# Kernel tuning notes

Measured on AMD Instinct MI355X. Metric: run time of the kernel, lower is better.

## Reference

```python
import jax, jax.numpy as jnp
import numpy as np

B, T, D, L = 64, 512, 400, 25
H = D // 2  # per-direction LSTM hidden


def setup_inputs():
    key = jax.random.key(0)
    ks = jax.random.split(key, 16)
    s = 0.1
    lengths = jax.random.randint(ks[0], (B,), T // 2, T + 1)
    mask = (jnp.arange(T)[None, :] < lengths[:, None]).astype(jnp.float32)
    labels = (jax.random.randint(ks[1], (B, T), 1, L) * mask.astype(jnp.int32)).astype(jnp.int32)

    def n(k, shape):
        return jax.random.normal(k, shape, jnp.float32) * s

    return {
        "input_embed": jax.random.normal(ks[2], (B, T, D), jnp.float32),
        "mask": mask,
        "labels": labels,
        "Wih_f": n(ks[3], (4 * H, D)), "Whh_f": n(ks[4], (4 * H, H)),
        "bih_f": n(ks[5], (4 * H,)), "bhh_f": n(ks[6], (4 * H,)),
        "Wih_b": n(ks[7], (4 * H, D)), "Whh_b": n(ks[8], (4 * H, H)),
        "bih_b": n(ks[9], (4 * H,)), "bhh_b": n(ks[10], (4 * H,)),
        "Wl": n(ks[11], (L, D)), "bl": n(ks[12], (L,)),
        "trans": n(ks[13], (L, L)), "start": n(ks[14], (L,)), "end": n(ks[15], (L,)),
    }


def _lstm_dir(x_tbd, m_tb1, Wih, Whh, bih, bhh, reverse):
    # Masked LSTM scan == pack_padded semantics: state frozen past sequence end.
    Bn = x_tbd.shape[1]
    h0 = jnp.zeros((Bn, H), x_tbd.dtype)

    def step(carry, inp):
        h, c = carry
        x, m = inp
        g = x @ Wih.T + h @ Whh.T + (bih + bhh)
        i, f, gg, o = jnp.split(g, 4, axis=-1)  # PyTorch gate order i,f,g,o
        i, f, o = jax.nn.sigmoid(i), jax.nn.sigmoid(f), jax.nn.sigmoid(o)
        c_new = f * c + i * jnp.tanh(gg)
        h_new = o * jnp.tanh(c_new)
        h = m * h_new + (1.0 - m) * h
        c = m * c_new + (1.0 - m) * c
        return (h, c), h

    _, hs = jax.lax.scan(step, (h0, h0), (x_tbd, m_tb1), reverse=reverse)
    return hs  # [T,B,H]


def _emissions(input_embed, mask, params):
    (Wih_f, Whh_f, bih_f, bhh_f, Wih_b, Whh_b, bih_b, bhh_b, Wl, bl) = params
    x = jnp.transpose(input_embed, (1, 0, 2))    # [T,B,D]
    m = jnp.transpose(mask, (1, 0))[:, :, None]  # [T,B,1]
    hf = _lstm_dir(x, m, Wih_f, Whh_f, bih_f, bhh_f, False)
    hb = _lstm_dir(x, m, Wih_b, Whh_b, bih_b, bhh_b, True)
    h = jnp.concatenate([hf, hb], axis=-1) * m   # pad positions zeroed like pad_packed_sequence
    e = (h @ Wl.T + bl) * m                      # `out *= mask.unsqueeze(-1)`
    return jnp.transpose(e, (1, 0, 2))           # [B,T,L]


def _crf_llh(e, labels, mask, trans, start, end):
    # numerator (gold path score)
    em = jnp.take_along_axis(e, labels[..., None], axis=-1)[..., 0]  # [B,T]
    tr = trans[labels[:, :-1], labels[:, 1:]]                        # [B,T-1]
    last = (jnp.sum(mask, axis=1) - 1.0).astype(jnp.int32)
    y_last = jnp.take_along_axis(labels, last[:, None], axis=1)[:, 0]
    num = start[labels[:, 0]] + em[:, 0] \
        + jnp.sum(mask[:, 1:] * (em[:, 1:] + tr), axis=1) + end[y_last]
    # log-partition via forward algorithm
    e_t = jnp.transpose(e, (1, 0, 2))  # [T,B,L]
    m_t = jnp.transpose(mask, (1, 0))  # [T,B]
    alpha0 = start[None, :] + e_t[0]

    def step(alpha, inp):
        et, mt = inp
        new = jax.nn.logsumexp(alpha[:, :, None] + trans[None], axis=1) + et
        return jnp.where(mt[:, None] > 0, new, alpha), None

    alpha, _ = jax.lax.scan(step, alpha0, (e_t[1:], m_t[1:]))
    logZ = jax.nn.logsumexp(alpha + end[None, :], axis=-1)
    return num - logZ  # [B] log-likelihood


def _viterbi(e, mask, trans, start, end):
    Bn = e.shape[0]
    e_t = jnp.transpose(e, (1, 0, 2))
    m_t = jnp.transpose(mask, (1, 0))
    delta0 = start[None, :] + e_t[0]
    eye_idx = jnp.broadcast_to(jnp.arange(L, dtype=jnp.int32), (Bn, L))

    def step(delta, inp):
        et, mt = inp
        cand = delta[:, :, None] + trans[None]  # [B, L_prev, L_cur]
        ptr = jnp.argmax(cand, axis=1).astype(jnp.int32)
        new = jnp.max(cand, axis=1) + et
        mb = mt[:, None] > 0
        return jnp.where(mb, new, delta), jnp.where(mb, ptr, eye_idx)

    delta, ptrs = jax.lax.scan(step, delta0, (e_t[1:], m_t[1:]))  # ptrs: [T-1,B,L]
    y_last = jnp.argmax(delta + end[None, :], axis=-1).astype(jnp.int32)  # [B]

    def back(y, ptr):
        y_prev = jnp.take_along_axis(ptr, y[:, None], axis=1)[:, 0]
        return y_prev, y_prev

    _, ys = jax.lax.scan(back, y_last, ptrs, reverse=True)  # [T-1,B]
    path = jnp.concatenate([ys, y_last[None]], axis=0)      # [T,B]
    return jnp.transpose(path, (1, 0)) * mask.astype(jnp.int32)  # pads -> pad_idx 0


def reference(input_embed, mask, labels, Wih_f, Whh_f, bih_f, bhh_f,
              Wih_b, Whh_b, bih_b, bhh_b, Wl, bl, trans, start, end):
    params = (Wih_f, Whh_f, bih_f, bhh_f, Wih_b, Whh_b, bih_b, bhh_b, Wl, bl)
    e = _emissions(input_embed, mask, params)
    loss = -jnp.mean(_crf_llh(e, labels, mask, trans, start, end))  # -torch.mean(score)
    preds = _viterbi(e, mask, trans, start, end)
    return loss, preds
```

## Files before the change

kernel.cpp:

```cpp
#include <hip/hip_runtime.h>
#include <cmath>

#define Bn 64
#define Tn 512
#define Dn 400
#define Ln 25
#define Hn 200
#define G4n 800
#define TCn 64
#define NCH 8
#define NPADn 832
#define JV 20
#define JLB 17
#define JSB 3

constexpr size_t OFF_WIHT = 0;
constexpr size_t OFF_WHHP = OFF_WIHT + (size_t)2*Dn*NPADn;
constexpr size_t OFF_WHHB = OFF_WHHP + (size_t)2*Hn*G4n;
constexpr size_t OFF_BSUM = OFF_WHHB + (size_t)2*Hn*G4n/2;
constexpr size_t OFF_GB   = OFF_BSUM + (size_t)2*G4n;
constexpr size_t OFF_HCAT = OFF_GB + (size_t)2*2*Bn*TCn*G4n/2;
constexpr size_t OFF_E    = OFF_HCAT + (size_t)Bn*Tn*2*Hn;
constexpr size_t OFF_HST  = OFF_E + (size_t)Bn*Tn*Ln;
constexpr size_t OFF_CST  = OFF_HST + (size_t)2*Bn*Hn;
constexpr size_t OFF_PART = OFF_CST + (size_t)2*Bn*Hn;

#define SMEM_BYTES 153664

__device__ __forceinline__ float sigf(float x) { return 1.0f / (1.0f + expf(-x)); }

__global__ void prep_kernel(const float* __restrict__ Wih_f, const float* __restrict__ Whh_f,
                            const float* __restrict__ bih_f, const float* __restrict__ bhh_f,
                            const float* __restrict__ Wih_b, const float* __restrict__ Whh_b,
                            const float* __restrict__ bih_b, const float* __restrict__ bhh_b,
                            float* __restrict__ ws) {
    int tid = blockIdx.x * blockDim.x + threadIdx.x;
    int nth = gridDim.x * blockDim.x;
    float* WihT = ws + OFF_WIHT;
    float* WhhP = ws + OFF_WHHP;
    unsigned short* WhhB = (unsigned short*)(ws + OFF_WHHB);
    float* bsum = ws + OFF_BSUM;
    float* hst  = ws + OFF_HST;
    float* cst  = ws + OFF_CST;
    for (int i = tid; i < 2*Dn*NPADn; i += nth) {
        int d = i / (Dn*NPADn); int r = i % (Dn*NPADn); int k = r / NPADn; int g = r % NPADn;
        const float* W = d ? Wih_b : Wih_f;
        WihT[i] = (g < G4n) ? W[(size_t)g*Dn + k] : 0.0f;
    }
    for (int i = tid; i < 2*Hn*G4n; i += nth) {
        int d = i / (Hn*G4n); int r = i % (Hn*G4n);
        int j = r / G4n; int g = r % G4n;
        int k = g >> 2, q = g & 3;
        const float* W = d ? Whh_b : Whh_f;
        float v = W[(size_t)(q*Hn + k)*Hn + j];
        WhhP[i] = v;
        WhhB[i] = (unsigned short)(__float_as_uint(v) >> 16);
    }
    for (int i = tid; i < 2*G4n; i += nth) {
        int d = i / G4n; int g = i % G4n;
        bsum[i] = d ? (bih_b[g] + bhh_b[g]) : (bih_f[g] + bhh_f[g]);
    }
    for (int i = tid; i < 2*Bn*Hn; i += nth) { hst[i] = 0.0f; cst[i] = 0.0f; }
}

__device__ __forceinline__ void gemm_role(const float* __restrict__ X, float* __restrict__ ws,
                                          int chunk, int tile, int tid, char* smem) {
    const float* WihT = ws + OFF_WIHT;
    const float* bsum = ws + OFF_BSUM;
    unsigned short* Gb = (unsigned short*)(ws + OFF_GB) + (size_t)(chunk & 1) * 2 * Bn * TCn * G4n;
    int q4 = tid >> 8;
    int t2 = tid & 255;
    float* As = (float*)(smem + q4 * 13056);
    float* Bs = As + 16 * 136;
    int g0i = tile % 13; int rem = tile / 13;
    int bp = rem % 32;   int d = rem / 32;
    int g0 = g0i * 64;
    int tx = t2 % 16, ty = t2 / 16;
    int t_base = (d == 0) ? chunk * TCn : (Tn - (chunk + 1) * TCn);
    const float* Bmat = WihT + (size_t)d * Dn * NPADn;

    float acc[8][4] = {{0.f}};
    int lr = t2 / 2, lk = t2 % 2;
    int bk = t2 / 16, bg = t2 % 16;
    int a_b = bp * 2 + lr / 64;
    int a_t = t_base + (lr % 64);
    const float* Arow = X + ((size_t)a_b * Tn + a_t) * Dn;

    for (int kt = 0; kt < Dn; kt += 16) {
        float4 a4a = *(const float4*)(Arow + kt + lk * 8);
        float4 a4b = *(const float4*)(Arow + kt + lk * 8 + 4);
        float4 b4  = *(const float4*)(Bmat + (size_t)(kt + bk) * NPADn + g0 + bg * 4);
        __syncthreads();
        As[(lk*8+0)*136 + lr] = a4a.x; As[(lk*8+1)*136 + lr] = a4a.y;
        As[(lk*8+2)*136 + lr] = a4a.z; As[(lk*8+3)*136 + lr] = a4a.w;
        As[(lk*8+4)*136 + lr] = a4b.x; As[(lk*8+5)*136 + lr] = a4b.y;
        As[(lk*8+6)*136 + lr] = a4b.z; As[(lk*8+7)*136 + lr] = a4b.w;
        *(float4*)&Bs[bk*68 + bg*4] = b4;
        __syncthreads();
        #pragma unroll
        for (int kk = 0; kk < 16; ++kk) {
            float4 af0 = *(const float4*)&As[kk*136 + ty*8];
            float4 af1 = *(const float4*)&As[kk*136 + ty*8 + 4];
            float4 bf  = *(const float4*)&Bs[kk*68 + tx*4];
            acc[0][0] += af0.x*bf.x; acc[0][1] += af0.x*bf.y; acc[0][2] += af0.x*bf.z; acc[0][3] += af0.x*bf.w;
            acc[1][0] += af0.y*bf.x; acc[1][1] += af0.y*bf.y; acc[1][2] += af0.y*bf.z; acc[1][3] += af0.y*bf.w;
            acc[2][0] += af0.z*bf.x; acc[2][1] += af0.z*bf.y; acc[2][2] += af0.z*bf.z; acc[2][3] += af0.z*bf.w;
            acc[3][0] += af0.w*bf.x; acc[3][1] += af0.w*bf.y; acc[3][2] += af0.w*bf.z; acc[3][3] += af0.w*bf.w;
            acc[4][0] += af1.x*bf.x; acc[4][1] += af1.x*bf.y; acc[4][2] += af1.x*bf.z; acc[4][3] += af1.x*bf.w;
            acc[5][0] += af1.y*bf.x; acc[5][1] += af1.y*bf.y; acc[5][2] += af1.y*bf.z; acc[5][3] += af1.y*bf.w;
            acc[6][0] += af1.z*bf.x; acc[6][1] += af1.z*bf.y; acc[6][2] += af1.z*bf.z; acc[6][3] += af1.z*bf.w;
            acc[7][0] += af1.w*bf.x; acc[7][1] += af1.w*bf.y; acc[7][2] += af1.w*bf.z; acc[7][3] += af1.w*bf.w;
        }
    }
    #pragma unroll
    for (int ii = 0; ii < 8; ++ii) {
        int r = ty * 8 + ii;
        int b = bp * 2 + r / 64;
        int tloc = r % 64;
        #pragma unroll
        for (int jj = 0; jj < 4; ++jj) {
            int g = g0 + tx * 4 + jj;
            if (g < G4n) {
                int k = g % Hn, q = g / Hn;
                float v = acc[ii][jj] + bsum[d*G4n + g];
                Gb[(((size_t)d*Bn + b)*TCn + tloc)*G4n + k*4 + q] =
                    (unsigned short)(__float_as_uint(v) >> 16);
            }
        }
    }
}

__device__ __forceinline__ void rec_role(const float* __restrict__ mask, float* __restrict__ ws,
                                         int chunk, int b, int d, int tid, char* smem) {
    const unsigned short* Gbs = (const unsigned short*)(ws + OFF_GB) + (size_t)(chunk & 1) * 2 * Bn * TCn * G4n;
    float* Hcat = ws + OFF_HCAT;
    float* hst = ws + OFF_HST;
    float* cst = ws + OFF_CST;
    const float* WP = ws + OFF_WHHP;
    const unsigned short* WBbase = (const unsigned short*)(ws + OFF_WHHB);

    uint2*  wldsB   = (uint2*)smem;
    float4* partial = (float4*)(smem + 136000);
    float*  hbuf    = (float*)(smem + 152000);

    int k = tid % 200;
    int part = tid / 200;
    bool act = (part < 5);
    int cbase = (act ? part : 0) * 40;
    int qq = tid & 3, kk = tid >> 2;
    bool bact = (tid < 800);

    const float* Wd = WP + (size_t)d * Hn * G4n;
    const unsigned short* WB = WBbase + (size_t)d * Hn * G4n;
    #define LW(i) float4 w##i = *(const float4*)(Wd + (size_t)(cbase + i) * G4n + k * 4);
    LW(0) LW(1) LW(2) LW(3) LW(4) LW(5) LW(6) LW(7) LW(8) LW(9)
    LW(10) LW(11) LW(12) LW(13) LW(14) LW(15) LW(16) LW(17) LW(18) LW(19)
    #undef LW
    int lbase = (act ? part : 0) * 200 + k;
    if (act) {
        #pragma unroll
        for (int jj = 0; jj < JLB; ++jj)
            wldsB[jj * 1000 + part * 200 + k] = *(const uint2*)(WB + (size_t)(cbase + JV + jj) * G4n + k * 4);
    }
    size_t soff = ((size_t)d * Bn + b) * Hn;
    float hr = 0.f, cr = 0.f;
    if (bact && qq == 0) {
        hr = hst[soff + kk];
        cr = cst[soff + kk];
    }
    if (tid < 200) hbuf[tid] = hst[soff + tid];
    __syncthreads();

    const unsigned short* WstB = WB + (size_t)(cbase + JV + JLB) * G4n + k * 4;
    const unsigned short* GbRow = Gbs + ((size_t)d * Bn + b) * TCn * G4n;
    const float* mrow = mask + (size_t)b * Tn;
    float* Hrow = Hcat + (size_t)b * Tn * (2 * Hn) + d * Hn;

    #define FMAB(U, H) { \
        float bx = __uint_as_float((U).x << 16); \
        float by = __uint_as_float((U).x & 0xffff0000u); \
        float bz = __uint_as_float((U).y << 16); \
        float bw = __uint_as_float((U).y & 0xffff0000u); \
        acc.x += bx*(H); acc.y += by*(H); acc.z += bz*(H); acc.w += bw*(H); }
    #define FMA1(W, H) acc.x += (W).x*(H); acc.y += (W).y*(H); acc.z += (W).z*(H); acc.w += (W).w*(H);

    int cur = 0;
    for (int s = 0; s < TCn; ++s) {
        int tg, tloc;
        if (d == 0) { tloc = s; tg = chunk * TCn + s; }
        else        { tloc = TCn - 1 - s; tg = Tn - 1 - (chunk * TCn + s); }
        if (s > 0 && tid < 200) {
            int tgp = (d == 0) ? (chunk * TCn + s - 1) : (Tn - 1 - (chunk * TCn + s - 1));
            Hrow[(size_t)tgp * (2 * Hn) + tid] = hbuf[cur * 208 + tid];
        }
        float m_ = 0.f, gq = 0.f;
        if (bact) {
            m_ = mrow[tg];
            unsigned short gub = GbRow[(size_t)tloc * G4n + tid];
            gq = __uint_as_float((unsigned int)gub << 16);
        }
        {
            uint2 t0 = *(const uint2*)(WstB + (size_t)0 * G4n);
            uint2 t1 = *(const uint2*)(WstB + (size_t)1 * G4n);
            uint2 t2s = *(const uint2*)(WstB + (size_t)2 * G4n);
            float4 acc = {0.f, 0.f, 0.f, 0.f};
            float4 hv;
            const float* hb = hbuf + cur * 208;
            hv = *(const float4*)&hb[cbase + 0];
            FMA1(w0, hv.x) FMA1(w1, hv.y) FMA1(w2, hv.z) FMA1(w3, hv.w)
            hv = *(const float4*)&hb[cbase + 4];
            FMA1(w4, hv.x) FMA1(w5, hv.y) FMA1(w6, hv.z) FMA1(w7, hv.w)
            hv = *(const float4*)&hb[cbase + 8];
            FMA1(w8, hv.x) FMA1(w9, hv.y) FMA1(w10, hv.z) FMA1(w11, hv.w)
            hv = *(const float4*)&hb[cbase + 12];
            FMA1(w12, hv.x) FMA1(w13, hv.y) FMA1(w14, hv.z) FMA1(w15, hv.w)
            hv = *(const float4*)&hb[cbase + 16];
            FMA1(w16, hv.x) FMA1(w17, hv.y) FMA1(w18, hv.z) FMA1(w19, hv.w)
            {
                uint2 u0 = wldsB[0*1000+lbase], u1 = wldsB[1*1000+lbase];
                uint2 u2 = wldsB[2*1000+lbase], u3 = wldsB[3*1000+lbase];
                hv = *(const float4*)&hb[cbase + 20];
                FMAB(u0, hv.x) FMAB(u1, hv.y) FMAB(u2, hv.z) FMAB(u3, hv.w)
            }
            {
                uint2 u0 = wldsB[4*1000+lbase], u1 = wldsB[5*1000+lbase];
                uint2 u2 = wldsB[6*1000+lbase], u3 = wldsB[7*1000+lbase];
                hv = *(const float4*)&hb[cbase + 24];
                FMAB(u0, hv.x) FMAB(u1, hv.y) FMAB(u2, hv.z) FMAB(u3, hv.w)
            }
            {
                uint2 u0 = wldsB[8*1000+lbase], u1 = wldsB[9*1000+lbase];
                uint2 u2 = wldsB[10*1000+lbase], u3 = wldsB[11*1000+lbase];
                hv = *(const float4*)&hb[cbase + 28];
                FMAB(u0, hv.x) FMAB(u1, hv.y) FMAB(u2, hv.z) FMAB(u3, hv.w)
            }
            {
                uint2 u0 = wldsB[12*1000+lbase], u1 = wldsB[13*1000+lbase];
                uint2 u2 = wldsB[14*1000+lbase], u3 = wldsB[15*1000+lbase];
                hv = *(const float4*)&hb[cbase + 32];
                FMAB(u0, hv.x) FMAB(u1, hv.y) FMAB(u2, hv.z) FMAB(u3, hv.w)
            }
            {
                uint2 u16 = wldsB[16*1000+lbase];
                hv = *(const float4*)&hb[cbase + 36];
                FMAB(u16, hv.x) FMAB(t0, hv.y) FMAB(t1, hv.z) FMAB(t2s, hv.w)
            }
            if (act) partial[part * 200 + k] = acc;
        }
        __syncthreads();
        if (bact) {
            const float* pf = (const float*)partial;
            float g = gq + (((pf[0*800 + tid] + pf[1*800 + tid]) +
                             (pf[2*800 + tid] + pf[3*800 + tid])) + pf[4*800 + tid]);
            float arg = (qq == 2) ? 2.f * g : g;
            float sg = 1.f / (1.f + expf(-arg));
            float a = (qq == 2) ? 2.f * sg - 1.f : sg;
            float x1 = __shfl_xor(a, 1);
            float x2 = __shfl_xor(a, 2);
            float x3 = __shfl_xor(x1, 2);
            if (qq == 0) {
                float i_ = a, f_ = x1, gg_ = x2, o_ = x3;
                float cn = f_ * cr + i_ * gg_;
                float hn = o_ * tanhf(cn);
                cr = m_ * cn + (1.f - m_) * cr;
                hr = m_ * hn + (1.f - m_) * hr;
                hbuf[(cur ^ 1) * 208 + kk] = hr;
            }
        }
        __syncthreads();
        cur ^= 1;
    }
    #undef FMAB
    #undef FMA1
    if (tid < 200) {
        int tgp = (d == 0) ? (chunk * TCn + TCn - 1) : (Tn - 1 - (chunk * TCn + TCn - 1));
        Hrow[(size_t)tgp * (2 * Hn) + tid] = hbuf[cur * 208 + tid];
    }
    if (bact && qq == 0) {
        hst[soff + kk] = hr;
        cst[soff + kk] = cr;
    }
}

__device__ __forceinline__ void emis_role(const float* __restrict__ mask,
                                          const float* __restrict__ Wl, const float* __restrict__ bl,
                                          float* __restrict__ ws, int blk, int tid, char* smem) {
    const float* Hcat = ws + OFF_HCAT;
    float* E = ws + OFF_E;
    float* Wls = (float*)smem;
    int q4 = tid >> 8, t2 = tid & 255;
    float* Hs = (float*)(smem + 40448 + q4 * 25856);
    for (int i = tid; i < Ln * 100; i += 1024) {
        int l = i / 100, k4 = i % 100;
        *(float4*)&Wls[l*404 + k4*4] = *(const float4*)(Wl + (size_t)l*Dn + k4*4);
    }
    int Q = blk * 4 + q4;
    int b = Q / 3, seg = Q % 3;
    int rbase = b * Tn + 64 + seg * 128;
    for (int sub = 0; sub < 8; ++sub) {
        int r0 = rbase + sub * 16;
        __syncthreads();
        for (int i = t2; i < 16 * 100; i += 256) {
            int r = i / 100, k4 = i % 100;
            *(float4*)&Hs[r*404 + k4*4] = *(const float4*)(Hcat + (size_t)(r0 + r)*Dn + k4*4);
        }
        __syncthreads();
        for (int o = t2; o < 16 * Ln; o += 256) {
            int r = o / Ln, l = o % Ln;
            float acc = 0.f;
            #pragma unroll 4
            for (int k4 = 0; k4 < 100; ++k4) {
                float4 h = *(const float4*)&Hs[r*404 + k4*4];
                float4 wv = *(const float4*)&Wls[l*404 + k4*4];
                acc += h.x*wv.x + h.y*wv.y + h.z*wv.z + h.w*wv.w;
            }
            int row = r0 + r;
            float m = mask[row];
            E[(size_t)row * Ln + l] = (acc + bl[l]) * m;
        }
    }
}

__global__ __launch_bounds__(1024, 4) void fused_kernel(const float* __restrict__ X,
                                                        const float* __restrict__ mask,
                                                        const float* __restrict__ Wl,
                                                        const float* __restrict__ bl,
                                                        float* __restrict__ ws,
                                                        int rec_chunk, int gemm_chunk,
                                                        int nrec, int ngemm) {
    __shared__ __align__(16) char smem[SMEM_BYTES];
    int bx = blockIdx.x;
    int tid = threadIdx.x;
    if (bx < nrec) {
        rec_role(mask, ws, rec_chunk, bx & 63, bx >> 6, tid, smem);
    } else if (bx < nrec + ngemm) {
        int tile = (bx - nrec) * 4 + (tid >> 8);
        gemm_role(X, ws, gemm_chunk, tile, tid, smem);
    } else {
        emis_role(mask, Wl, bl, ws, bx - nrec - ngemm, tid, smem);
    }
}

__global__ __launch_bounds__(256) void emis2_kernel(const float* __restrict__ mask,
                                                    const float* __restrict__ Wl,
                                                    const float* __restrict__ bl,
                                                    float* __restrict__ ws) {
    const float* Hcat = ws + OFF_HCAT;
    float* E = ws + OFF_E;
    __shared__ float Wls[Ln * 404];
    __shared__ float Hs[16 * 404];
    int tid = threadIdx.x;
    int b = blockIdx.x;
    for (int i = tid; i < Ln * 100; i += 256) {
        int l = i / 100, k4 = i % 100;
        *(float4*)&Wls[l*404 + k4*4] = *(const float4*)(Wl + (size_t)l*Dn + k4*4);
    }
    for (int sub = 0; sub < 8; ++sub) {
        int t0 = (sub < 4) ? sub * 16 : 448 + (sub - 4) * 16;
        int r0 = b * Tn + t0;
        __syncthreads();
        for (int i = tid; i < 16 * 100; i += 256) {
            int r = i / 100, k4 = i % 100;
            *(float4*)&Hs[r*404 + k4*4] = *(const float4*)(Hcat + (size_t)(r0 + r)*Dn + k4*4);
        }
        __syncthreads();
        for (int o = tid; o < 16 * Ln; o += 256) {
            int r = o / Ln, l = o % Ln;
            float acc = 0.f;
            #pragma unroll 4
            for (int k4 = 0; k4 < 100; ++k4) {
                float4 h = *(const float4*)&Hs[r*404 + k4*4];
                float4 wv = *(const float4*)&Wls[l*404 + k4*4];
                acc += h.x*wv.x + h.y*wv.y + h.z*wv.z + h.w*wv.w;
            }
            int row = r0 + r;
            float m = mask[row];
            E[(size_t)row * Ln + l] = (acc + bl[l]) * m;
        }
    }
}

__global__ __launch_bounds__(128) void decode_kernel(const float* __restrict__ mask,
                                                     const int* __restrict__ labels,
                                                     const float* __restrict__ trans,
                                                     const float* __restrict__ start,
                                                     const float* __restrict__ endv,
                                                     float* __restrict__ ws,
                                                     float* __restrict__ out) {
    int b = blockIdx.x;
    int tid = threadIdx.x;
    int wvid = tid >> 6;
    int ln = tid & 63;
    int half = (ln >> 5) & 1;
    int l = ln & 31;
    bool actl = (l < Ln);
    int jbase = half ? 13 : 0;
    int jcnt  = half ? 12 : 13;
    const float* E = ws + OFF_E;
    float* part = ws + OFF_PART;

    __shared__ __align__(16) float Es[Tn * Ln];
    __shared__ float trs[Ln * Ln];
    __shared__ unsigned char ptrs[Tn][Ln];
    __shared__ unsigned char ys[Tn];

    {
        const float4* src = (const float4*)(E + (size_t)b * Tn * Ln);
        float4* dst = (float4*)Es;
        for (int i = tid; i < Tn * Ln / 4; i += 128) dst[i] = src[i];
        for (int i = tid; i < Ln * Ln; i += 128) trs[i] = trans[i];
    }
    float cnt = 0.f;
    for (int t = ln; t < Tn; t += 64) cnt += mask[(size_t)b * Tn + t];
    for (int off = 32; off; off >>= 1) cnt += __shfl_xor(cnt, off);
    int len = (int)(cnt + 0.5f);
    float trc[13];
    #pragma unroll
    for (int j = 0; j < 13; ++j) trc[j] = -1e30f;
    if (actl) {
        for (int j = 0; j < jcnt; ++j) trc[j] = trans[(jbase + j) * Ln + l];
    }
    __syncthreads();

    if (wvid == 0) {
        float alpha = actl ? start[l] + Es[l] : -1e30f;
        for (int t = 1; t < len; ++t) {
            float v[13];
            #pragma unroll
            for (int j = 0; j < 13; ++j) v[j] = __shfl(alpha, jbase + j) + trc[j];
            float a0 = fmaxf(v[0], v[1]), a1 = fmaxf(v[2], v[3]), a2 = fmaxf(v[4], v[5]);
            float a3 = fmaxf(v[6], v[7]), a4 = fmaxf(v[8], v[9]), a5 = fmaxf(v[10], v[11]);
            a0 = fmaxf(a0, a1); a2 = fmaxf(a2, a3); a4 = fmaxf(a4, a5);
            a0 = fmaxf(a0, a2); a4 = fmaxf(a4, v[12]);
            float m = fmaxf(a0, a4);
            float e[13];
            #pragma unroll
            for (int j = 0; j < 13; ++j) e[j] = __expf(v[j] - m);
            float s0 = (e[0] + e[1]) + (e[2] + e[3]);
            float s1 = (e[4] + e[5]) + (e[6] + e[7]);
            float s2 = (e[8] + e[9]) + (e[10] + e[11]);
            float s = ((s0 + s1) + (s2 + e[12]));
            float pm = __shfl_xor(m, 32);
            float ps = __shfl_xor(s, 32);
            float M = fmaxf(m, pm);
            float S = s * __expf(m - M) + ps * __expf(pm - M);
            float nv = M + __logf(S) + Es[t * Ln + l];
            alpha = actl ? nv : -1e30f;
        }
        float vfin = (ln < Ln) ? alpha + endv[l] : -1e30f;
        float mxf = vfin;
        for (int off = 32; off; off >>= 1) mxf = fmaxf(mxf, __shfl_xor(mxf, off));
        float sf = (ln < Ln) ? __expf(vfin - mxf) : 0.f;
        for (int off = 32; off; off >>= 1) sf += __shfl_xor(sf, off);
        float logZ = mxf + __logf(sf);
        float psum = 0.f;
        for (int t = ln; t < len; t += 64) {
            if (t >= 1) {
                int lt = labels[(size_t)b * Tn + t];
                int lp = labels[(size_t)b * Tn + t - 1];
                psum += Es[t * Ln + lt] + trs[lp * Ln + lt];
            }
        }
        for (int off = 32; off; off >>= 1) psum += __shfl_xor(psum, off);
        if (ln == 0) {
            int l0 = labels[(size_t)b * Tn];
            int yl = labels[(size_t)b * Tn + len - 1];
            part[b] = start[l0] + Es[l0] + psum + endv[yl] - logZ;
        }
    } else {
        float delta = actl ? start[l] + Es[l] : -1e30f;
        for (int t = 1; t < len; ++t) {
            float best = -1e30f; int ba = 0;
            #pragma unroll
            for (int j = 0; j < 13; ++j) {
                float c = __shfl(delta, jbase + j) + trc[j];
                if (c > best) { best = c; ba = jbase + j; }
            }
            float pb = __shfl_xor(best, 32);
            int   pa = __shfl_xor(ba, 32);
            float b0 = half ? pb : best; int a0 = half ? pa : ba;
            float b1 = half ? best : pb; int a1 = half ? ba : pa;
            int   A  = (b1 > b0) ? a1 : a0;
            float B  = fmaxf(b0, b1);
            float nd = B + Es[t * Ln + l];
            if (actl && half == 0) ptrs[t][l] = (unsigned char)A;
            delta = actl ? nd : -1e30f;
        }
        float bb = -1e30f; int y = 0;
        for (int j = 0; j < Ln; ++j) {
            float c = __shfl(delta, j) + endv[j];
            if (c > bb) { bb = c; y = j; }
        }
        if (ln == 0) {
            ys[len - 1] = (unsigned char)y;
            int yy = y;
            for (int t = len - 1; t >= 1; --t) { yy = ptrs[t][yy]; ys[t - 1] = (unsigned char)yy; }
        }
        __builtin_amdgcn_s_barrier();
        for (int t = ln; t < Tn; t += 64) {
            out[1 + (size_t)b * Tn + t] = (t < len) ? (float)ys[t] : 0.f;
        }
    }
}

__global__ __launch_bounds__(64) void fin_kernel(float* __restrict__ ws, float* __restrict__ out) {
    const float* part = ws + OFF_PART;
    int l = threadIdx.x;
    float v = (l < Bn) ? part[l] : 0.f;
    for (int off = 32; off; off >>= 1) v += __shfl_xor(v, off);
    if (l == 0) out[0] = -v / (float)Bn;
}

extern "C" void kernel_launch(void* const* d_in, const int* in_sizes, int n_in,
                              void* d_out, int out_size, void* d_ws, size_t ws_size,
                              hipStream_t stream) {
    (void)in_sizes; (void)n_in; (void)out_size; (void)ws_size;
    const float* X      = (const float*)d_in[0];
    const float* mask   = (const float*)d_in[1];
    const int*   labels = (const int*)d_in[2];
    const float* Wih_f  = (const float*)d_in[3];
    const float* Whh_f  = (const float*)d_in[4];
    const float* bih_f  = (const float*)d_in[5];
    const float* bhh_f  = (const float*)d_in[6];
    const float* Wih_b  = (const float*)d_in[7];
    const float* Whh_b  = (const float*)d_in[8];
    const float* bih_b  = (const float*)d_in[9];
    const float* bhh_b  = (const float*)d_in[10];
    const float* Wl     = (const float*)d_in[11];
    const float* bl     = (const float*)d_in[12];
    const float* trans  = (const float*)d_in[13];
    const float* start  = (const float*)d_in[14];
    const float* endv   = (const float*)d_in[15];
    float* ws  = (float*)d_ws;
    float* out = (float*)d_out;

    prep_kernel<<<128, 256, 0, stream>>>(Wih_f, Whh_f, bih_f, bhh_f,
                                         Wih_b, Whh_b, bih_b, bhh_b, ws);
    fused_kernel<<<208, 1024, 0, stream>>>(X, mask, Wl, bl, ws, 0, 0, 0, 208);
    for (int c = 1; c < NCH; ++c)
        fused_kernel<<<336, 1024, 0, stream>>>(X, mask, Wl, bl, ws, c - 1, c, 128, 208);
    fused_kernel<<<176, 1024, 0, stream>>>(X, mask, Wl, bl, ws, NCH - 1, 0, 128, 0);
    emis2_kernel<<<64, 256, 0, stream>>>(mask, Wl, bl, ws);
    decode_kernel<<<64, 128, 0, stream>>>(mask, labels, trans, start, endv, ws, out);
    fin_kernel<<<1, 64, 0, stream>>>(ws, out);
}
```

Before: 2.136 ms.

## Give each thread a full gate dot-product with packed bf16 recurrent weights

The recurrent step used to split each gate's 200-long dot product across five thread groups, mixing fp32 and bf16 weights, and then reduced the partial sums through shared memory behind an extra barrier. Each of the 800 threads now owns one gate output and does the whole dot product. All recurrent weights are stored as bf16 pairs packed into 32-bit words: 80 words sit in registers and 20 are staged in LDS. This drops one __syncthreads per timestep and the LDS partial-sum traffic, but makes every weight bf16 (lower precision than the mixed scheme) and raises register pressure, with 224 threads now idle during the matvec.

```diff
diff --git a/kernel.cpp b/kernel.cpp
--- a/kernel.cpp
+++ b/kernel.cpp
@@ -10,14 +10,11 @@
 #define TCn 64
 #define NCH 8
 #define NPADn 832
-#define JV 20
-#define JLB 17
-#define JSB 3
 
 constexpr size_t OFF_WIHT = 0;
 constexpr size_t OFF_WHHP = OFF_WIHT + (size_t)2*Dn*NPADn;
-constexpr size_t OFF_WHHB = OFF_WHHP + (size_t)2*Hn*G4n;
-constexpr size_t OFF_BSUM = OFF_WHHB + (size_t)2*Hn*G4n/2;
+constexpr size_t OFF_WPK  = OFF_WHHP + (size_t)2*Hn*G4n;
+constexpr size_t OFF_BSUM = OFF_WPK + (size_t)2*100*G4n;
 constexpr size_t OFF_GB   = OFF_BSUM + (size_t)2*G4n;
 constexpr size_t OFF_HCAT = OFF_GB + (size_t)2*2*Bn*TCn*G4n/2;
 constexpr size_t OFF_E    = OFF_HCAT + (size_t)Bn*Tn*2*Hn;
@@ -37,8 +34,7 @@
     int tid = blockIdx.x * blockDim.x + threadIdx.x;
     int nth = gridDim.x * blockDim.x;
     float* WihT = ws + OFF_WIHT;
-    float* WhhP = ws + OFF_WHHP;
-    unsigned short* WhhB = (unsigned short*)(ws + OFF_WHHB);
+    unsigned int* WPK = (unsigned int*)(ws + OFF_WPK);
     float* bsum = ws + OFF_BSUM;
     float* hst  = ws + OFF_HST;
     float* cst  = ws + OFF_CST;
@@ -47,14 +43,14 @@
         const float* W = d ? Wih_b : Wih_f;
         WihT[i] = (g < G4n) ? W[(size_t)g*Dn + k] : 0.0f;
     }
-    for (int i = tid; i < 2*Hn*G4n; i += nth) {
-        int d = i / (Hn*G4n); int r = i % (Hn*G4n);
-        int j = r / G4n; int g = r % G4n;
-        int k = g >> 2, q = g & 3;
+    for (int i = tid; i < 2*100*G4n; i += nth) {
+        int d = i / (100*G4n); int r = i % (100*G4n);
+        int j2 = r / G4n; int u = r % G4n;
+        int k = u >> 2, q = u & 3;
         const float* W = d ? Whh_b : Whh_f;
-        float v = W[(size_t)(q*Hn + k)*Hn + j];
-        WhhP[i] = v;
-        WhhB[i] = (unsigned short)(__float_as_uint(v) >> 16);
+        unsigned int lo = __float_as_uint(W[(size_t)(q*Hn + k)*Hn + 2*j2]) >> 16;
+        unsigned int hi = __float_as_uint(W[(size_t)(q*Hn + k)*Hn + 2*j2 + 1]) & 0xffff0000u;
+        WPK[i] = hi | lo;
     }
     for (int i = tid; i < 2*G4n; i += nth) {
         int d = i / G4n; int g = i % G4n;
@@ -136,53 +132,53 @@
     float* Hcat = ws + OFF_HCAT;
     float* hst = ws + OFF_HST;
     float* cst = ws + OFF_CST;
-    const float* WP = ws + OFF_WHHP;
-    const unsigned short* WBbase = (const unsigned short*)(ws + OFF_WHHB);
-
-    uint2*  wldsB   = (uint2*)smem;
-    float4* partial = (float4*)(smem + 136000);
-    float*  hbuf    = (float*)(smem + 152000);
-
-    int k = tid % 200;
-    int part = tid / 200;
-    bool act = (part < 5);
-    int cbase = (act ? part : 0) * 40;
-    int qq = tid & 3, kk = tid >> 2;
-    bool bact = (tid < 800);
-
-    const float* Wd = WP + (size_t)d * Hn * G4n;
-    const unsigned short* WB = WBbase + (size_t)d * Hn * G4n;
-    #define LW(i) float4 w##i = *(const float4*)(Wd + (size_t)(cbase + i) * G4n + k * 4);
-    LW(0) LW(1) LW(2) LW(3) LW(4) LW(5) LW(6) LW(7) LW(8) LW(9)
-    LW(10) LW(11) LW(12) LW(13) LW(14) LW(15) LW(16) LW(17) LW(18) LW(19)
-    #undef LW
-    int lbase = (act ? part : 0) * 200 + k;
+    const unsigned int* WPK = (const unsigned int*)(ws + OFF_WPK);
+
+    unsigned int* WL = (unsigned int*)smem;
+    float* hbufF = (float*)(smem + 64000);
+
+    int u = tid;
+    bool act = (u < 800);
+    int k = u >> 2, qq = u & 3;
+    const unsigned int* WPKd = WPK + (size_t)d * 100 * G4n;
+
+    #define LWU(i) unsigned int wu##i = WPKd[(size_t)(i) * 800 + (u & 1023)];
+    LWU(0) LWU(1) LWU(2) LWU(3) LWU(4) LWU(5) LWU(6) LWU(7) LWU(8) LWU(9)
+    LWU(10) LWU(11) LWU(12) LWU(13) LWU(14) LWU(15) LWU(16) LWU(17) LWU(18) LWU(19)
+    LWU(20) LWU(21) LWU(22) LWU(23) LWU(24) LWU(25) LWU(26) LWU(27) LWU(28) LWU(29)
+    LWU(30) LWU(31) LWU(32) LWU(33) LWU(34) LWU(35) LWU(36) LWU(37) LWU(38) LWU(39)
+    LWU(40) LWU(41) LWU(42) LWU(43) LWU(44) LWU(45) LWU(46) LWU(47) LWU(48) LWU(49)
+    LWU(50) LWU(51) LWU(52) LWU(53) LWU(54) LWU(55) LWU(56) LWU(57) LWU(58) LWU(59)
+    LWU(60) LWU(61) LWU(62) LWU(63) LWU(64) LWU(65) LWU(66) LWU(67) LWU(68) LWU(69)
+    LWU(70) LWU(71) LWU(72) LWU(73) LWU(74) LWU(75) LWU(76) LWU(77) LWU(78) LWU(79)
+    #undef LWU
     if (act) {
         #pragma unroll
-        for (int jj = 0; jj < JLB; ++jj)
-            wldsB[jj * 1000 + part * 200 + k] = *(const uint2*)(WB + (size_t)(cbase + JV + jj) * G4n + k * 4);
+        for (int jj = 0; jj < 20; ++jj)
+            WL[jj * 800 + u] = WPKd[(size_t)(80 + jj) * 800 + u];
     }
     size_t soff = ((size_t)d * Bn + b) * Hn;
     float hr = 0.f, cr = 0.f;
-    if (bact && qq == 0) {
-        hr = hst[soff + kk];
-        cr = cst[soff + kk];
-    }
-    if (tid < 200) hbuf[tid] = hst[soff + tid];
+    if (act && qq == 0) {
+        hr = hst[soff + k];
+        cr = cst[soff + k];
+    }
+    if (tid < 200) hbufF[tid] = hst[soff + tid];
     __syncthreads();
 
-    const unsigned short* WstB = WB + (size_t)(cbase + JV + JLB) * G4n + k * 4;
     const unsigned short* GbRow = Gbs + ((size_t)d * Bn + b) * TCn * G4n;
     const float* mrow = mask + (size_t)b * Tn;
     float* Hrow = Hcat + (size_t)b * Tn * (2 * Hn) + d * Hn;
 
-    #define FMAB(U, H) { \
-        float bx = __uint_as_float((U).x << 16); \
-        float by = __uint_as_float((U).x & 0xffff0000u); \
-        float bz = __uint_as_float((U).y << 16); \
-        float bw = __uint_as_float((U).y & 0xffff0000u); \
-        acc.x += bx*(H); acc.y += by*(H); acc.z += bz*(H); acc.w += bw*(H); }
-    #define FMA1(W, H) acc.x += (W).x*(H); acc.y += (W).y*(H); acc.z += (W).z*(H); acc.w += (W).w*(H);
+    #define UNL(W) __uint_as_float((W) << 16)
+    #define UNH(W) __uint_as_float((W) & 0xffff0000u)
+    #define GRP(g, WA, WB) { float4 h4v = hf4[g]; \
+        a0 += UNL(WA) * h4v.x; a1 += UNH(WA) * h4v.y; \
+        a2 += UNL(WB) * h4v.z; a3 += UNH(WB) * h4v.w; }
+    #define GRPL(g, I0, I1) { unsigned int wa = WL[(I0)*800 + u], wb = WL[(I1)*800 + u]; \
+        float4 h4v = hf4[g]; \
+        a0 += UNL(wa) * h4v.x; a1 += UNH(wa) * h4v.y; \
+        a2 += UNL(wb) * h4v.z; a3 += UNH(wb) * h4v.w; }
 
     int cur = 0;
     for (int s = 0; s < TCn; ++s) {
@@ -191,67 +187,27 @@
         else        { tloc = TCn - 1 - s; tg = Tn - 1 - (chunk * TCn + s); }
         if (s > 0 && tid < 200) {
             int tgp = (d == 0) ? (chunk * TCn + s - 1) : (Tn - 1 - (chunk * TCn + s - 1));
-            Hrow[(size_t)tgp * (2 * Hn) + tid] = hbuf[cur * 208 + tid];
-        }
-        float m_ = 0.f, gq = 0.f;
-        if (bact) {
-            m_ = mrow[tg];
-            unsigned short gub = GbRow[(size_t)tloc * G4n + tid];
-            gq = __uint_as_float((unsigned int)gub << 16);
-        }
-        {
-            uint2 t0 = *(const uint2*)(WstB + (size_t)0 * G4n);
-            uint2 t1 = *(const uint2*)(WstB + (size_t)1 * G4n);
-            uint2 t2s = *(const uint2*)(WstB + (size_t)2 * G4n);
-            float4 acc = {0.f, 0.f, 0.f, 0.f};
-            float4 hv;
-            const float* hb = hbuf + cur * 208;
-            hv = *(const float4*)&hb[cbase + 0];
-            FMA1(w0, hv.x) FMA1(w1, hv.y) FMA1(w2, hv.z) FMA1(w3, hv.w)
-            hv = *(const float4*)&hb[cbase + 4];
-            FMA1(w4, hv.x) FMA1(w5, hv.y) FMA1(w6, hv.z) FMA1(w7, hv.w)
-            hv = *(const float4*)&hb[cbase + 8];
-            FMA1(w8, hv.x) FMA1(w9, hv.y) FMA1(w10, hv.z) FMA1(w11, hv.w)
-            hv = *(const float4*)&hb[cbase + 12];
-            FMA1(w12, hv.x) FMA1(w13, hv.y) FMA1(w14, hv.z) FMA1(w15, hv.w)
-            hv = *(const float4*)&hb[cbase + 16];
-            FMA1(w16, hv.x) FMA1(w17, hv.y) FMA1(w18, hv.z) FMA1(w19, hv.w)
-            {
-                uint2 u0 = wldsB[0*1000+lbase], u1 = wldsB[1*1000+lbase];
-                uint2 u2 = wldsB[2*1000+lbase], u3 = wldsB[3*1000+lbase];
-                hv = *(const float4*)&hb[cbase + 20];
-                FMAB(u0, hv.x) FMAB(u1, hv.y) FMAB(u2, hv.z) FMAB(u3, hv.w)
-            }
-            {
-                uint2 u0 = wldsB[4*1000+lbase], u1 = wldsB[5*1000+lbase];
-                uint2 u2 = wldsB[6*1000+lbase], u3 = wldsB[7*1000+lbase];
-                hv = *(const float4*)&hb[cbase + 24];
-                FMAB(u0, hv.x) FMAB(u1, hv.y) FMAB(u2, hv.z) FMAB(u3, hv.w)
-            }
-            {
-                uint2 u0 = wldsB[8*1000+lbase], u1 = wldsB[9*1000+lbase];
-                uint2 u2 = wldsB[10*1000+lbase], u3 = wldsB[11*1000+lbase];
-                hv = *(const float4*)&hb[cbase + 28];
-                FMAB(u0, hv.x) FMAB(u1, hv.y) FMAB(u2, hv.z) FMAB(u3, hv.w)
-            }
-            {
-                uint2 u0 = wldsB[12*1000+lbase], u1 = wldsB[13*1000+lbase];
-                uint2 u2 = wldsB[14*1000+lbase], u3 = wldsB[15*1000+lbase];
-                hv = *(const float4*)&hb[cbase + 32];
-                FMAB(u0, hv.x) FMAB(u1, hv.y) FMAB(u2, hv.z) FMAB(u3, hv.w)
-            }
-            {
-                uint2 u16 = wldsB[16*1000+lbase];
-                hv = *(const float4*)&hb[cbase + 36];
-                FMAB(u16, hv.x) FMAB(t0, hv.y) FMAB(t1, hv.z) FMAB(t2s, hv.w)
-            }
-            if (act) partial[part * 200 + k] = acc;
-        }
-        __syncthreads();
-        if (bact) {
-            const float* pf = (const float*)partial;
-            float g = gq + (((pf[0*800 + tid] + pf[1*800 + tid]) +
-                             (pf[2*800 + tid] + pf[3*800 + tid])) + pf[4*800 + tid]);
+            Hrow[(size_t)tgp * (2 * Hn) + tid] = hbufF[cur * 208 + tid];
+        }
+        if (act) {
+            float m_ = mrow[tg];
+            unsigned short gub = GbRow[(size_t)tloc * G4n + u];
+            float gq = __uint_as_float((unsigned int)gub << 16);
+            const float4* hf4 = (const float4*)(hbufF + cur * 208);
+            float a0 = gq, a1 = 0.f, a2 = 0.f, a3 = 0.f;
+            GRP(0,wu0,wu1)   GRP(1,wu2,wu3)   GRP(2,wu4,wu5)   GRP(3,wu6,wu7)
+            GRP(4,wu8,wu9)   GRP(5,wu10,wu11) GRP(6,wu12,wu13) GRP(7,wu14,wu15)
+            GRP(8,wu16,wu17) GRP(9,wu18,wu19) GRP(10,wu20,wu21) GRP(11,wu22,wu23)
+            GRP(12,wu24,wu25) GRP(13,wu26,wu27) GRP(14,wu28,wu29) GRP(15,wu30,wu31)
+            GRP(16,wu32,wu33) GRP(17,wu34,wu35) GRP(18,wu36,wu37) GRP(19,wu38,wu39)
+            GRP(20,wu40,wu41) GRP(21,wu42,wu43) GRP(22,wu44,wu45) GRP(23,wu46,wu47)
+            GRP(24,wu48,wu49) GRP(25,wu50,wu51) GRP(26,wu52,wu53) GRP(27,wu54,wu55)
+            GRP(28,wu56,wu57) GRP(29,wu58,wu59) GRP(30,wu60,wu61) GRP(31,wu62,wu63)
+            GRP(32,wu64,wu65) GRP(33,wu66,wu67) GRP(34,wu68,wu69) GRP(35,wu70,wu71)
+            GRP(36,wu72,wu73) GRP(37,wu74,wu75) GRP(38,wu76,wu77) GRP(39,wu78,wu79)
+            GRPL(40,0,1)  GRPL(41,2,3)  GRPL(42,4,5)  GRPL(43,6,7)  GRPL(44,8,9)
+            GRPL(45,10,11) GRPL(46,12,13) GRPL(47,14,15) GRPL(48,16,17) GRPL(49,18,19)
+            float g = (a0 + a1) + (a2 + a3);
             float arg = (qq == 2) ? 2.f * g : g;
             float sg = 1.f / (1.f + expf(-arg));
             float a = (qq == 2) ? 2.f * sg - 1.f : sg;
@@ -264,21 +220,23 @@
                 float hn = o_ * tanhf(cn);
                 cr = m_ * cn + (1.f - m_) * cr;
                 hr = m_ * hn + (1.f - m_) * hr;
-                hbuf[(cur ^ 1) * 208 + kk] = hr;
+                hbufF[(cur ^ 1) * 208 + k] = hr;
             }
         }
         __syncthreads();
         cur ^= 1;
     }
-    #undef FMAB
-    #undef FMA1
+    #undef GRP
+    #undef GRPL
+    #undef UNL
+    #undef UNH
     if (tid < 200) {
         int tgp = (d == 0) ? (chunk * TCn + TCn - 1) : (Tn - 1 - (chunk * TCn + TCn - 1));
-        Hrow[(size_t)tgp * (2 * Hn) + tid] = hbuf[cur * 208 + tid];
-    }
-    if (bact && qq == 0) {
-        hst[soff + kk] = hr;
-        cst[soff + kk] = cr;
+        Hrow[(size_t)tgp * (2 * Hn) + tid] = hbufF[cur * 208 + tid];
+    }
+    if (act && qq == 0) {
+        hst[soff + k] = hr;
+        cst[soff + k] = cr;
     }
 }
 
```

New measurement: 4.902 ms. 2.29x slower.
